# Kernel tuning notes

Measured on AMD Instinct MI355X. Metric: run time of the kernel, lower is better.

## Reference

```python
import jax, jax.numpy as jnp
import numpy as np

MAX_ITER = 10   # float32 branch of cg()
TOL = 1e-10

def _cdot(a, b):
    # complex_dot: sum(conj(a) * b) over all elements
    return jnp.sum(jnp.conj(a) * b)

def _A(p, smaps, mask):
    # p: [H,W] complex, smaps: [C,H,W] complex, mask: [H,W] real
    return jnp.fft.fft2(smaps * p[None], norm='ortho') * mask[None]

def _AH(y, smaps, mask):
    imgs = jnp.fft.ifft2(y * mask[None], norm='ortho')
    return jnp.sum(jnp.conj(smaps) * imgs, axis=0)  # [H,W]

def _cg(M, rhs):
    # conjugate gradient, faithful to the TF while_loop body
    def cond(s):
        i, rTr, x, r, p = s
        return jnp.logical_and(i < MAX_ITER, rTr > TOL)
    def body(s):
        i, rTr, x, r, p = s
        Ap = M(p)
        alpha = rTr / jnp.real(_cdot(p, Ap))
        x = x + p * alpha
        r = r - Ap * alpha
        rTrNew = jnp.real(_cdot(r, r))
        beta = rTrNew / rTr
        p = r + p * beta
        return (i + 1, rTrNew, x, r, p)
    rTr0 = jnp.real(_cdot(rhs, rhs))
    s0 = (jnp.int32(0), rTr0, jnp.zeros_like(rhs), rhs, rhs)
    return jax.lax.while_loop(cond, body, s0)[2]

def _solve_one(lambdaa, rhs, smaps, mask):
    M = lambda p: _AH(_A(p, smaps, mask), smaps, mask) + p * lambdaa
    return _cg(M, rhs)

_solve_b = jax.vmap(_solve_one, in_axes=(None, 0, 0, 0))  # replaces map_fn
_AH_b = jax.vmap(_AH, in_axes=(0, 0, 0))

def setup_inputs():
    key = jax.random.key(0)
    ks = jax.random.split(key, 7)
    B, C, H, W = 4, 16, 384, 384
    f = lambda k, s: jax.random.normal(k, s, dtype=jnp.float32)
    return {
        'lambdaa': 0.05 * jnp.ones((), jnp.float32),
        'x_re': f(ks[0], (B, H, W)),
        'x_im': f(ks[1], (B, H, W)),
        'y_re': f(ks[2], (B, C, H, W)),
        'y_im': f(ks[3], (B, C, H, W)),
        'smaps_re': f(ks[4], (B, C, H, W)),
        'smaps_im': f(ks[5], (B, C, H, W)),
        'mask': (jax.random.uniform(ks[6], (B, H, W)) < 0.33).astype(jnp.float32),
    }

def reference(lambdaa, x_re, x_im, y_re, y_im, smaps_re, smaps_im, mask):
    x = jax.lax.complex(x_re, x_im)
    y = jax.lax.complex(y_re, y_im)
    smaps = jax.lax.complex(smaps_re, smaps_im)
    # rhs = AH(y) + lambdaa * x
    rhs = _AH_b(y, smaps, mask) + x * lambdaa
    out = _solve_b(lambdaa, rhs, smaps, mask)  # [B,H,W] complex
    return jnp.stack([out.real, out.imag], axis=-1)  # [B,H,W,2] float32
```

## Files before the change

kernel.cpp:

```cpp
#include <hip/hip_runtime.h>
#include <hip/hip_fp16.h>


#define Bn 4
#define Cn 16
#define Hn 384
#define Wn 384
#define NPIX (Hn*Wn)
#define NPIX2 (NPIX/2)
#define TPB 256
#define CTPB 512
#define NCOL 16
#define TOLF 1e-10f
#define NITER 10
#define RED_BLKS 72
#define RPITCH 416
#define CPITCH 417

__device__ __forceinline__ float2 cadd(float2 a, float2 b){ return make_float2(a.x+b.x, a.y+b.y); }
__device__ __forceinline__ float2 csub(float2 a, float2 b){ return make_float2(a.x-b.x, a.y-b.y); }
__device__ __forceinline__ float2 cmulf(float2 a, float2 b){
  return make_float2(a.x*b.x - a.y*b.y, a.x*b.y + a.y*b.x);
}

__device__ __forceinline__ void wave_fence(){ asm volatile("s_waitcnt lgkmcnt(0)" ::: "memory"); }

template<int IMM>
__device__ __forceinline__ float2 shx(float2 v){
  int x = __builtin_amdgcn_ds_swizzle(__float_as_int(v.x), IMM);
  int y = __builtin_amdgcn_ds_swizzle(__float_as_int(v.y), IMM);
  return make_float2(__int_as_float(x), __int_as_float(y));
}

__device__ __forceinline__ int rev5(int x){
  return ((x&1)<<4) | ((x&2)<<2) | (x&4) | ((x&8)>>2) | ((x&16)>>4);
}

__device__ __forceinline__ int offmap(int w){ return w + ((w*683)>>13); }

template<int DIR>
__device__ __forceinline__ void fft12(float2* v)
{
  const float S3 = (DIR<0) ? -0.86602540378443864676f : 0.86602540378443864676f;
  const float sg = (DIR<0) ? -1.f : 1.f;
  float2 t[4][3];
#pragma unroll
  for (int b = 0; b < 4; ++b) {
    float2 a0 = v[b], a1 = v[4+b], a2 = v[8+b];
    float2 s = cadd(a1,a2), d = csub(a1,a2);
    float2 mm = make_float2(a0.x - 0.5f*s.x, a0.y - 0.5f*s.y);
    float2 e  = make_float2(-d.y*S3, d.x*S3);
    t[b][0] = cadd(a0,s);
    t[b][1] = cadd(mm,e);
    t[b][2] = csub(mm,e);
  }
  const float2 w1  = make_float2(0.86602540378443864676f, sg*0.5f);
  const float2 w2  = make_float2(0.5f, sg*0.86602540378443864676f);
  const float2 w3  = make_float2(0.f, sg);
  const float2 w4t = make_float2(-0.5f, sg*0.86602540378443864676f);
  const float2 w6  = make_float2(-1.f, 0.f);
  t[1][1] = cmulf(t[1][1], w1);  t[1][2] = cmulf(t[1][2], w2);
  t[2][1] = cmulf(t[2][1], w2);  t[2][2] = cmulf(t[2][2], w4t);
  t[3][1] = cmulf(t[3][1], w3);  t[3][2] = cmulf(t[3][2], w6);
#pragma unroll
  for (int c = 0; c < 3; ++c) {
    float2 e = cadd(t[0][c], t[2][c]);
    float2 f = csub(t[0][c], t[2][c]);
    float2 g = cadd(t[1][c], t[3][c]);
    float2 h = csub(t[1][c], t[3][c]);
    float2 ih = (DIR<0) ? make_float2(h.y, -h.x) : make_float2(-h.y, h.x);
    v[c]   = cadd(e,g);
    v[c+3] = cadd(f,ih);
    v[c+6] = csub(e,g);
    v[c+9] = csub(f,ih);
  }
}

template<int DIR>
__device__ __forceinline__ void fft32_lanes(float2* v, int li)
{
  const float c2pi = (DIR<0) ? -6.2831853071795864769f : 6.2831853071795864769f;
  const float sg   = (DIR<0) ? -1.f : 1.f;
  float s, c;
  __sincosf(c2pi*(1.f/32.f)*(float)(li&15), &s, &c); float2 wA = make_float2(c,s);
  __sincosf(c2pi*(1.f/16.f)*(float)(li&7),  &s, &c); float2 wB = make_float2(c,s);
  __sincosf(c2pi*(1.f/ 8.f)*(float)(li&3),  &s, &c); float2 wC = make_float2(c,s);
  bool bA = li & 16, bB = li & 8, bC = li & 4, bD = li & 2, bE = li & 1;
#pragma unroll
  for (int k = 0; k < 12; ++k) {
    float2 a = v[k], o;
    o = shx<0x401F>(a); a = bA ? cmulf(csub(o,a), wA) : cadd(a,o);
    o = shx<0x201F>(a); a = bB ? cmulf(csub(o,a), wB) : cadd(a,o);
    o = shx<0x101F>(a); a = bC ? cmulf(csub(o,a), wC) : cadd(a,o);
    o = shx<0x081F>(a);
    { float2 su = cadd(a,o), d = csub(o,a);
      float2 dw = bE ? make_float2(-sg*d.y, sg*d.x) : d;
      a = bD ? dw : su; }
    o = shx<0x041F>(a); a = bE ? csub(o,a) : cadd(a,o);
    v[k] = a;
  }
}

template<int DIR>
__device__ __forceinline__ void fft384(float2* v, int li)
{
  fft12<DIR>(v);
  const float c2pi = (DIR<0) ? -6.2831853071795864769f : 6.2831853071795864769f;
  float s, c;
  __sincosf(c2pi*(1.f/384.f)*(float)li, &s, &c);
  float2 W = make_float2(c,s), cw = W;
#pragma unroll
  for (int k = 1; k < 12; ++k) { v[k] = cmulf(v[k], cw); cw = cmulf(cw, W); }
  fft32_lanes<DIR>(v, li);
}


__global__ __launch_bounds__(TPB) void k_row_fwd(
    const float2* __restrict__ p, const float* __restrict__ Sre,
    const float* __restrict__ Sim, __half2* __restrict__ tmp)
{
  __shared__ float2 lbuf[8*RPITCH];
  int tid = threadIdx.x;
  int wave = tid>>6, lane = tid&63, sub = lane>>5, li = lane&31;
  int row = wave*2 + sub;
  int tile = blockIdx.x % (Hn/8);
  int bc   = blockIdx.x / (Hn/8);
  int b = bc / Cn;
  int h = tile*8 + row;
  size_t gbase = (size_t)bc*NPIX + (size_t)h*Wn;
  size_t pbase = (size_t)b*NPIX + (size_t)h*Wn;

  float2 v[12];
#pragma unroll
  for (int k = 0; k < 12; ++k) {
    int w = 32*k + li;
    float2 pv = p[pbase + w];
    float sr = Sre[gbase + w], si = Sim[gbase + w];
    v[k] = make_float2(sr*pv.x - si*pv.y, sr*pv.y + si*pv.x);
  }
  fft384<-1>(v, li);
  int m = rev5(li);
  float2* lrow = lbuf + row*RPITCH;
#pragma unroll
  for (int k = 0; k < 12; ++k) lrow[13*m + k] = v[k];
  wave_fence();
#pragma unroll
  for (int k = 0; k < 12; ++k) {
    int w = 32*k + li;
    tmp[gbase + w] = __float22half2_rn(lrow[offmap(w)]);
  }
}

template<int CPGt>
__global__ __launch_bounds__(TPB) void k_row_inv_acc(
    const __half2* __restrict__ tmp, const float* __restrict__ Sre,
    const float* __restrict__ Sim, float2* __restrict__ partial)
{
  const int GRPt = Cn/CPGt;
  __shared__ float2 lbuf[8*RPITCH];
  int tid = threadIdx.x;
  int wave = tid>>6, lane = tid&63, sub = lane>>5, li = lane&31;
  int row = wave*2 + sub;
  int tile = blockIdx.x % (Hn/8);
  int rest = blockIdx.x / (Hn/8);
  int g = rest % GRPt;
  int b = rest / GRPt;
  int h = tile*8 + row;
  int m = rev5(li);
  float2* lrow = lbuf + row*RPITCH;

  size_t gbase0 = ((size_t)b*Cn + g*CPGt)*NPIX + (size_t)h*Wn;
  __half2 hb[12];
#pragma unroll
  for (int k = 0; k < 12; ++k) hb[k] = tmp[gbase0 + 32*k + li];

  float2 acc[12];
#pragma unroll
  for (int k = 0; k < 12; ++k) acc[k] = make_float2(0.f, 0.f);

  for (int j = 0; j < CPGt; ++j) {
    size_t gb = gbase0 + (size_t)j*NPIX;
    float2 vc[12];
#pragma unroll
    for (int k = 0; k < 12; ++k) vc[k] = __half22float2(hb[k]);
    if (j + 1 < CPGt) {
      size_t gbn = gb + NPIX;
#pragma unroll
      for (int k = 0; k < 12; ++k) hb[k] = tmp[gbn + 32*k + li];
    }
    fft384<1>(vc, li);
    wave_fence();
#pragma unroll
    for (int k = 0; k < 12; ++k) lrow[13*m + k] = vc[k];
    wave_fence();
#pragma unroll
    for (int k = 0; k < 12; ++k) {
      int w = 32*k + li;
      float2 u = lrow[offmap(w)];
      float sr = Sre[gb + w], si = Sim[gb + w];
      acc[k].x += sr*u.x + si*u.y;
      acc[k].y += sr*u.y - si*u.x;
    }
  }
  size_t pbase = ((size_t)g*Bn + b)*NPIX + (size_t)h*Wn;
#pragma unroll
  for (int k = 0; k < 12; ++k) partial[pbase + 32*k + li] = acc[k];
}

__global__ __launch_bounds__(TPB) void k_maskp(
    const float* __restrict__ mask, float* __restrict__ maskP,
    float* __restrict__ scal)
{
  int idx = blockIdx.x*TPB + threadIdx.x;
  if (blockIdx.x == 0) scal[threadIdx.x] = 0.0f;
  if (idx >= Bn*NPIX) return;
  int k = idx % 12; int t = idx / 12;
  int li = t & 31; t >>= 5;
  int w = t % Wn;  int b = t / Wn;
  maskP[idx] = mask[((size_t)b*Hn + (k + 12*rev5(li)))*Wn + w] * (1.0f/(float)NPIX);
}

__global__ __launch_bounds__(CTPB) void k_col_full(
    __half2* __restrict__ tmp, const float* __restrict__ maskP)
{
  __shared__ float2 dbuf[NCOL*CPITCH];
  int tid = threadIdx.x;
  int wave = tid>>6, lane = tid&63, sub = lane>>5, li = lane&31;
  int col = wave*2 + sub;
  int tile = blockIdx.x % (Wn/NCOL);
  int bc   = blockIdx.x / (Wn/NCOL);
  int b = bc / Cn;
  int w0 = tile*NCOL;
  size_t tbase = (size_t)bc*NPIX;

  for (int e = tid; e < NCOL*Hn; e += CTPB) {
    int wi = e & (NCOL-1), h = e >> 4;
    dbuf[wi*CPITCH + offmap(h)] = __half22float2(tmp[tbase + (size_t)h*Wn + w0 + wi]);
  }
  __syncthreads();

  float2* drow = dbuf + col*CPITCH;
  int w = w0 + col;
  int m = rev5(li);
  const float4* mp4 = (const float4*)(maskP + (((size_t)b*Wn + w)*32 + li)*12);
  float4 m0 = mp4[0], m1 = mp4[1], m2 = mp4[2];
  float2 v[12];
#pragma unroll
  for (int k = 0; k < 12; ++k) v[k] = drow[offmap(32*k + li)];
  fft384<-1>(v, li);
  float mk[12] = {m0.x,m0.y,m0.z,m0.w, m1.x,m1.y,m1.z,m1.w, m2.x,m2.y,m2.z,m2.w};
#pragma unroll
  for (int k = 0; k < 12; ++k) v[k] = make_float2(v[k].x*mk[k], v[k].y*mk[k]);
  wave_fence();
#pragma unroll
  for (int k = 0; k < 12; ++k) drow[13*m + k] = v[k];
  wave_fence();
#pragma unroll
  for (int k = 0; k < 12; ++k) v[k] = drow[offmap(32*k + li)];
  fft384<1>(v, li);
  wave_fence();
#pragma unroll
  for (int k = 0; k < 12; ++k) drow[13*m + k] = v[k];
  __syncthreads();

  for (int e = tid; e < NCOL*Hn; e += CTPB) {
    int wi = e & (NCOL-1), h = e >> 4;
    tmp[tbase + (size_t)h*Wn + w0 + wi] = __float22half2_rn(dbuf[wi*CPITCH + offmap(h)]);
  }
}

__global__ __launch_bounds__(CTPB) void k_col_rhs(
    const float* __restrict__ yre, const float* __restrict__ yim,
    const float* __restrict__ mask, __half2* __restrict__ tmp)
{
  __shared__ float2 dbuf[NCOL*CPITCH];
  int tid = threadIdx.x;
  int wave = tid>>6, lane = tid&63, sub = lane>>5, li = lane&31;
  int col = wave*2 + sub;
  int tile = blockIdx.x % (Wn/NCOL);
  int bc   = blockIdx.x / (Wn/NCOL);
  int b = bc / Cn;
  int w0 = tile*NCOL;
  size_t tbase = (size_t)bc*NPIX;
  size_t mbase = (size_t)b*NPIX;

  for (int e = tid; e < NCOL*Hn; e += CTPB) {
    int wi = e & (NCOL-1), h = e >> 4;
    size_t gi = (size_t)h*Wn + w0 + wi;
    float mv = mask[mbase + gi] * (1.0f/384.0f);
    dbuf[wi*CPITCH + offmap(h)] = make_float2(yre[tbase+gi]*mv, yim[tbase+gi]*mv);
  }
  __syncthreads();

  float2* drow = dbuf + col*CPITCH;
  int m = rev5(li);
  float2 v[12];
#pragma unroll
  for (int k = 0; k < 12; ++k) v[k] = drow[offmap(32*k + li)];
  fft384<1>(v, li);
  wave_fence();
#pragma unroll
  for (int k = 0; k < 12; ++k) drow[13*m + k] = v[k];
  __syncthreads();

  for (int e = tid; e < NCOL*Hn; e += CTPB) {
    int wi = e & (NCOL-1), h = e >> 4;
    tmp[tbase + (size_t)h*Wn + w0 + wi] = __float22half2_rn(dbuf[wi*CPITCH + offmap(h)]);
  }
}


__device__ __forceinline__ void block_reduce_atomic(float sum, float* target)
{
  __shared__ float red[TPB];
  red[threadIdx.x] = sum; __syncthreads();
  for (int s = TPB/2; s > 0; s >>= 1) {
    if (threadIdx.x < s) red[threadIdx.x] += red[threadIdx.x + s];
    __syncthreads();
  }
  if (threadIdx.x == 0) unsafeAtomicAdd(target, red[0]);
  __syncthreads();
}

template<int GRPt>
__global__ __launch_bounds__(TPB) void k_rhs_init(
    const float* __restrict__ xre, const float* __restrict__ xim,
    const float* __restrict__ lam, const float2* __restrict__ partial,
    float2* __restrict__ r, float2* __restrict__ p, float2* __restrict__ x,
    float* __restrict__ scal)
{
  int b = blockIdx.y;
  float l = lam[0];
  float sum = 0.0f;
  const float2* xr2 = (const float2*)(xre + (size_t)b*NPIX);
  const float2* xi2 = (const float2*)(xim + (size_t)b*NPIX);
  float4* r4 = (float4*)(r + (size_t)b*NPIX);
  float4* p4 = (float4*)(p + (size_t)b*NPIX);
  float4* x4 = (float4*)(x + (size_t)b*NPIX);
  for (int i = blockIdx.x*TPB + threadIdx.x; i < NPIX2; i += RED_BLKS*TPB) {
    float2 re = xr2[i], im = xi2[i];
    float4 rv = make_float4(l*re.x, l*im.x, l*re.y, l*im.y);
#pragma unroll
    for (int g = 0; g < GRPt; ++g) {
      float4 pv = ((const float4*)(partial + ((size_t)g*Bn + b)*NPIX))[i];
      rv.x += pv.x; rv.y += pv.y; rv.z += pv.z; rv.w += pv.w;
    }
    r4[i] = rv; p4[i] = rv;
    x4[i] = make_float4(0.f, 0.f, 0.f, 0.f);
    sum += rv.x*rv.x + rv.y*rv.y + rv.z*rv.z + rv.w*rv.w;
  }
  block_reduce_atomic(sum, &scal[b]);
}

template<int GRPt>
__global__ __launch_bounds__(TPB) void k_combine_dot3(
    const float2* __restrict__ p, const float2* __restrict__ r,
    const float* __restrict__ lam, const float2* __restrict__ partial,
    float2* __restrict__ Ap, float* __restrict__ slot)
{
  int b = blockIdx.y;
  float l = lam[0];
  float s_pAp = 0.f, s_AA = 0.f, s_rA = 0.f;
  const float4* p4 = (const float4*)(p + (size_t)b*NPIX);
  const float4* r4 = (const float4*)(r + (size_t)b*NPIX);
  float4* A4 = (float4*)(Ap + (size_t)b*NPIX);
  for (int i = blockIdx.x*TPB + threadIdx.x; i < NPIX2; i += RED_BLKS*TPB) {
    float4 pv = p4[i];
    float4 av = make_float4(l*pv.x, l*pv.y, l*pv.z, l*pv.w);
#pragma unroll
    for (int g = 0; g < GRPt; ++g) {
      float4 qv = ((const float4*)(partial + ((size_t)g*Bn + b)*NPIX))[i];
      av.x += qv.x; av.y += qv.y; av.z += qv.z; av.w += qv.w;
    }
    A4[i] = av;
    float4 rv = r4[i];
    s_pAp += pv.x*av.x + pv.y*av.y + pv.z*av.z + pv.w*av.w;
    s_AA  += av.x*av.x + av.y*av.y + av.z*av.z + av.w*av.w;
    s_rA  += rv.x*av.x + rv.y*av.y + rv.z*av.z + rv.w*av.w;
  }
  block_reduce_atomic(s_pAp, &slot[b]);
  block_reduce_atomic(s_AA,  &slot[4+b]);
  block_reduce_atomic(s_rA,  &slot[8+b]);
}

__global__ void k_scal(float* __restrict__ scal, int it)
{
  int b = threadIdx.x;
  if (b >= Bn) return;
  float rtr = scal[it*4 + b];
  const float* slot = scal + 64 + it*12;
  float* ab = scal + 224 + it*12;
  bool act = rtr > TOLF;
  float alpha = act ? rtr / slot[b] : 0.f;
  float rtrn = act ? fmaxf(rtr - 2.f*alpha*slot[8+b] + alpha*alpha*slot[4+b], 0.f) : rtr;
  float beta = act ? rtrn / rtr : 0.f;
  scal[(it+1)*4 + b] = rtrn;
  ab[b] = alpha; ab[4+b] = beta; ab[8+b] = act ? 1.f : 0.f;
}

__global__ __launch_bounds__(TPB) void k_upd(
    float2* __restrict__ x, float2* __restrict__ r, float2* __restrict__ p,
    const float2* __restrict__ Ap, const float* __restrict__ ab)
{
  int b = blockIdx.y;
  if (!(ab[8+b] > 0.5f)) return;
  float alpha = ab[b], beta = ab[4+b];
  float4* x4 = (float4*)(x + (size_t)b*NPIX);
  float4* r4 = (float4*)(r + (size_t)b*NPIX);
  float4* p4 = (float4*)(p + (size_t)b*NPIX);
  const float4* A4 = (const float4*)(Ap + (size_t)b*NPIX);
  for (int i = blockIdx.x*TPB + threadIdx.x; i < NPIX2; i += RED_BLKS*TPB) {
    float4 pv = p4[i], av = A4[i], xv = x4[i], rv = r4[i];
    xv.x += alpha*pv.x; xv.y += alpha*pv.y; xv.z += alpha*pv.z; xv.w += alpha*pv.w;
    rv.x -= alpha*av.x; rv.y -= alpha*av.y; rv.z -= alpha*av.z; rv.w -= alpha*av.w;
    x4[i] = xv; r4[i] = rv;
    p4[i] = make_float4(rv.x + beta*pv.x, rv.y + beta*pv.y,
                        rv.z + beta*pv.z, rv.w + beta*pv.w);
  }
}


extern "C" void kernel_launch(void* const* d_in, const int* in_sizes, int n_in,
                              void* d_out, int out_size, void* d_ws, size_t ws_size,
                              hipStream_t stream)
{
  const float* lam  = (const float*)d_in[0];
  const float* xre  = (const float*)d_in[1];
  const float* xim  = (const float*)d_in[2];
  const float* yre  = (const float*)d_in[3];
  const float* yim  = (const float*)d_in[4];
  const float* sre  = (const float*)d_in[5];
  const float* sim  = (const float*)d_in[6];
  const float* mask = (const float*)d_in[7];

  const size_t szTmp  = (size_t)Bn*Cn*NPIX*sizeof(__half2);
  const size_t szVec  = (size_t)Bn*NPIX*sizeof(float2);
  const size_t szMask = (size_t)Bn*NPIX*sizeof(float);
  const size_t need8  = szTmp + 8*szVec + 3*szVec + 2048 + szMask;
  const int GRP = (ws_size >= need8) ? 8 : 4;

  char* ws = (char*)d_ws;
  __half2* tmp = (__half2*)ws;  ws += szTmp;
  float2* part = (float2*)ws;   ws += (size_t)GRP*szVec;
  float2* r    = (float2*)ws;   ws += szVec;
  float2* p    = (float2*)ws;   ws += szVec;
  float2* Ap   = (float2*)ws;   ws += szVec;
  float*  scal = (float*)ws;    ws += 2048;
  float*  mskP = (float*)ws;
  float2* x    = (float2*)d_out;

  dim3 blk(TPB);
  dim3 rg(RED_BLKS, Bn);
  int grid_row = Bn*Cn*(Hn/8);
  int grid_col = Bn*Cn*(Wn/NCOL);
  int grid_inv = Bn*GRP*(Hn/8);

  k_maskp<<<(Bn*NPIX)/TPB, blk, 0, stream>>>(mask, mskP, scal);

  k_col_rhs<<<grid_col, CTPB, 0, stream>>>(yre, yim, mask, tmp);
  if (GRP == 8) {
    k_row_inv_acc<2><<<grid_inv, blk, 0, stream>>>(tmp, sre, sim, part);
    k_rhs_init<8><<<rg, blk, 0, stream>>>(xre, xim, lam, part, r, p, x, scal);
  } else {
    k_row_inv_acc<4><<<grid_inv, blk, 0, stream>>>(tmp, sre, sim, part);
    k_rhs_init<4><<<rg, blk, 0, stream>>>(xre, xim, lam, part, r, p, x, scal);
  }

  for (int it = 0; it < NITER; ++it) {
    k_row_fwd<<<grid_row, blk, 0, stream>>>(p, sre, sim, tmp);
    k_col_full<<<grid_col, CTPB, 0, stream>>>(tmp, mskP);
    if (GRP == 8) {
      k_row_inv_acc<2><<<grid_inv, blk, 0, stream>>>(tmp, sre, sim, part);
      k_combine_dot3<8><<<rg, blk, 0, stream>>>(p, r, lam, part, Ap, scal + 64 + it*12);
    } else {
      k_row_inv_acc<4><<<grid_inv, blk, 0, stream>>>(tmp, sre, sim, part);
      k_combine_dot3<4><<<rg, blk, 0, stream>>>(p, r, lam, part, Ap, scal + 64 + it*12);
    }
    k_scal<<<1, 64, 0, stream>>>(scal, it);
    k_upd<<<rg, blk, 0, stream>>>(x, r, p, Ap, scal + 224 + it*12);
  }
}
```

Baseline: 1.580 ms.

## Keep CG-loop spectra in scrambled order and pack coil maps to half2

Inside the CG loop, the forward row FFT now writes its output in the FFT's natural scrambled order, with no LDS reorder. The column pass and the inverse row FFT then use a matching decimation-in-time FFT that accepts scrambled input and returns natural order. The mask permutation is adjusted to match the scrambled column index. This removes several LDS shuffles and fences per FFT. Separately, the coil sensitivity maps are packed once into a half2 buffer (when workspace allows) to halve their read traffic, at the cost of extra rounding error. Channel grouping is fixed at four groups instead of choosing eight when space allows.

```diff
diff --git a/kernel.cpp b/kernel.cpp
--- a/kernel.cpp
+++ b/kernel.cpp
@@ -14,6 +14,8 @@
 #define TOLF 1e-10f
 #define NITER 10
 #define RED_BLKS 72
+#define GRP 4
+#define CPG 4
 #define RPITCH 416
 #define CPITCH 417
 
@@ -102,6 +104,33 @@
 }
 
 template<int DIR>
+__device__ __forceinline__ void fft32_lanes_dit(float2* v, int li)
+{
+  const float c2pi = (DIR<0) ? -6.2831853071795864769f : 6.2831853071795864769f;
+  const float sg   = (DIR<0) ? -1.f : 1.f;
+  float s, c;
+  __sincosf(c2pi*(1.f/32.f)*(float)(li&15), &s, &c); float2 wA = make_float2(c,s);
+  __sincosf(c2pi*(1.f/16.f)*(float)(li&7),  &s, &c); float2 wB = make_float2(c,s);
+  __sincosf(c2pi*(1.f/ 8.f)*(float)(li&3),  &s, &c); float2 wC = make_float2(c,s);
+  bool bA = li & 16, bB = li & 8, bC = li & 4, bD = li & 2, bE = li & 1;
+#pragma unroll
+  for (int k = 0; k < 12; ++k) {
+    float2 a = v[k], o;
+    o = shx<0x041F>(a); a = bE ? csub(o,a) : cadd(a,o);
+    { float2 aw = make_float2(-sg*a.y, sg*a.x);
+      a = (bD && bE) ? aw : a;
+      o = shx<0x081F>(a); a = bD ? csub(o,a) : cadd(a,o); }
+    { float2 aw = cmulf(a, wC); a = bC ? aw : a;
+      o = shx<0x101F>(a); a = bC ? csub(o,a) : cadd(a,o); }
+    { float2 aw = cmulf(a, wB); a = bB ? aw : a;
+      o = shx<0x201F>(a); a = bB ? csub(o,a) : cadd(a,o); }
+    { float2 aw = cmulf(a, wA); a = bA ? aw : a;
+      o = shx<0x401F>(a); a = bA ? csub(o,a) : cadd(a,o); }
+    v[k] = a;
+  }
+}
+
+template<int DIR>
 __device__ __forceinline__ void fft384(float2* v, int li)
 {
   fft12<DIR>(v);
@@ -114,12 +143,26 @@
   fft32_lanes<DIR>(v, li);
 }
 
-
+template<int DIR>
+__device__ __forceinline__ void fft384_scr(float2* v, int li)
+{
+  fft32_lanes_dit<DIR>(v, li);
+  const float c2pi = (DIR<0) ? -6.2831853071795864769f : 6.2831853071795864769f;
+  float s, c;
+  __sincosf(c2pi*(1.f/384.f)*(float)li, &s, &c);
+  float2 W = make_float2(c,s), cw = W;
+#pragma unroll
+  for (int k = 1; k < 12; ++k) { v[k] = cmulf(v[k], cw); cw = cmulf(cw, W); }
+  fft12<DIR>(v);
+}
+
+
+template<bool HS>
 __global__ __launch_bounds__(TPB) void k_row_fwd(
     const float2* __restrict__ p, const float* __restrict__ Sre,
-    const float* __restrict__ Sim, __half2* __restrict__ tmp)
-{
-  __shared__ float2 lbuf[8*RPITCH];
+    const float* __restrict__ Sim, const __half2* __restrict__ Sh,
+    __half2* __restrict__ tmp)
+{
   int tid = threadIdx.x;
   int wave = tid>>6, lane = tid&63, sub = lane>>5, li = lane&31;
   int row = wave*2 + sub;
@@ -135,41 +178,84 @@
   for (int k = 0; k < 12; ++k) {
     int w = 32*k + li;
     float2 pv = p[pbase + w];
-    float sr = Sre[gbase + w], si = Sim[gbase + w];
+    float sr, si;
+    if (HS) { float2 sv = __half22float2(Sh[gbase + w]); sr = sv.x; si = sv.y; }
+    else    { sr = Sre[gbase + w]; si = Sim[gbase + w]; }
     v[k] = make_float2(sr*pv.x - si*pv.y, sr*pv.y + si*pv.x);
   }
   fft384<-1>(v, li);
-  int m = rev5(li);
-  float2* lrow = lbuf + row*RPITCH;
-#pragma unroll
-  for (int k = 0; k < 12; ++k) lrow[13*m + k] = v[k];
-  wave_fence();
-#pragma unroll
-  for (int k = 0; k < 12; ++k) {
-    int w = 32*k + li;
-    tmp[gbase + w] = __float22half2_rn(lrow[offmap(w)]);
-  }
-}
-
-template<int CPGt>
-__global__ __launch_bounds__(TPB) void k_row_inv_acc(
+#pragma unroll
+  for (int k = 0; k < 12; ++k)
+    tmp[gbase + 32*k + li] = __float22half2_rn(v[k]);
+}
+
+template<bool HS>
+__global__ __launch_bounds__(TPB) void k_row_inv_scr(
+    const __half2* __restrict__ tmp, const float* __restrict__ Sre,
+    const float* __restrict__ Sim, const __half2* __restrict__ Sh,
+    float2* __restrict__ partial)
+{
+  int tid = threadIdx.x;
+  int wave = tid>>6, lane = tid&63, sub = lane>>5, li = lane&31;
+  int row = wave*2 + sub;
+  int tile = blockIdx.x % (Hn/8);
+  int rest = blockIdx.x / (Hn/8);
+  int g = rest % GRP;
+  int b = rest / GRP;
+  int h = tile*8 + row;
+
+  size_t gbase0 = ((size_t)b*Cn + g*CPG)*NPIX + (size_t)h*Wn;
+  __half2 hb[12];
+#pragma unroll
+  for (int k = 0; k < 12; ++k) hb[k] = tmp[gbase0 + 32*k + li];
+
+  float2 acc[12];
+#pragma unroll
+  for (int k = 0; k < 12; ++k) acc[k] = make_float2(0.f, 0.f);
+
+  for (int j = 0; j < CPG; ++j) {
+    size_t gb = gbase0 + (size_t)j*NPIX;
+    float2 vc[12];
+#pragma unroll
+    for (int k = 0; k < 12; ++k) vc[k] = __half22float2(hb[k]);
+    if (j + 1 < CPG) {
+      size_t gbn = gb + NPIX;
+#pragma unroll
+      for (int k = 0; k < 12; ++k) hb[k] = tmp[gbn + 32*k + li];
+    }
+    fft384_scr<1>(vc, li);
+#pragma unroll
+    for (int k = 0; k < 12; ++k) {
+      int w = 32*k + li;
+      float sr, si;
+      if (HS) { float2 sv = __half22float2(Sh[gb + w]); sr = sv.x; si = sv.y; }
+      else    { sr = Sre[gb + w]; si = Sim[gb + w]; }
+      acc[k].x += sr*vc[k].x + si*vc[k].y;
+      acc[k].y += sr*vc[k].y - si*vc[k].x;
+    }
+  }
+  size_t pbase = ((size_t)g*Bn + b)*NPIX + (size_t)h*Wn;
+#pragma unroll
+  for (int k = 0; k < 12; ++k) partial[pbase + 32*k + li] = acc[k];
+}
+
+__global__ __launch_bounds__(TPB) void k_row_inv_nat(
     const __half2* __restrict__ tmp, const float* __restrict__ Sre,
     const float* __restrict__ Sim, float2* __restrict__ partial)
 {
-  const int GRPt = Cn/CPGt;
   __shared__ float2 lbuf[8*RPITCH];
   int tid = threadIdx.x;
   int wave = tid>>6, lane = tid&63, sub = lane>>5, li = lane&31;
   int row = wave*2 + sub;
   int tile = blockIdx.x % (Hn/8);
   int rest = blockIdx.x / (Hn/8);
-  int g = rest % GRPt;
-  int b = rest / GRPt;
+  int g = rest % GRP;
+  int b = rest / GRP;
   int h = tile*8 + row;
   int m = rev5(li);
   float2* lrow = lbuf + row*RPITCH;
 
-  size_t gbase0 = ((size_t)b*Cn + g*CPGt)*NPIX + (size_t)h*Wn;
+  size_t gbase0 = ((size_t)b*Cn + g*CPG)*NPIX + (size_t)h*Wn;
   __half2 hb[12];
 #pragma unroll
   for (int k = 0; k < 12; ++k) hb[k] = tmp[gbase0 + 32*k + li];
@@ -178,12 +264,12 @@
 #pragma unroll
   for (int k = 0; k < 12; ++k) acc[k] = make_float2(0.f, 0.f);
 
-  for (int j = 0; j < CPGt; ++j) {
+  for (int j = 0; j < CPG; ++j) {
     size_t gb = gbase0 + (size_t)j*NPIX;
     float2 vc[12];
 #pragma unroll
     for (int k = 0; k < 12; ++k) vc[k] = __half22float2(hb[k]);
-    if (j + 1 < CPGt) {
+    if (j + 1 < CPG) {
       size_t gbn = gb + NPIX;
 #pragma unroll
       for (int k = 0; k < 12; ++k) hb[k] = tmp[gbn + 32*k + li];
@@ -207,6 +293,14 @@
   for (int k = 0; k < 12; ++k) partial[pbase + 32*k + li] = acc[k];
 }
 
+__global__ __launch_bounds__(TPB) void k_spack(
+    const float* __restrict__ sre, const float* __restrict__ sim,
+    __half2* __restrict__ sh)
+{
+  size_t i = (size_t)blockIdx.x*TPB + threadIdx.x;
+  if (i < (size_t)Bn*Cn*NPIX) sh[i] = __floats2half2_rn(sre[i], sim[i]);
+}
+
 __global__ __launch_bounds__(TPB) void k_maskp(
     const float* __restrict__ mask, float* __restrict__ maskP,
     float* __restrict__ scal)
@@ -216,8 +310,9 @@
   if (idx >= Bn*NPIX) return;
   int k = idx % 12; int t = idx / 12;
   int li = t & 31; t >>= 5;
-  int w = t % Wn;  int b = t / Wn;
-  maskP[idx] = mask[((size_t)b*Hn + (k + 12*rev5(li)))*Wn + w] * (1.0f/(float)NPIX);
+  int wa = t % Wn; int b = t / Wn;
+  int wt = (wa >> 5) + 12*rev5(wa & 31);
+  maskP[idx] = mask[((size_t)b*Hn + (k + 12*rev5(li)))*Wn + wt] * (1.0f/(float)NPIX);
 }
 
 __global__ __launch_bounds__(CTPB) void k_col_full(
@@ -241,7 +336,6 @@
 
   float2* drow = dbuf + col*CPITCH;
   int w = w0 + col;
-  int m = rev5(li);
   const float4* mp4 = (const float4*)(maskP + (((size_t)b*Wn + w)*32 + li)*12);
   float4 m0 = mp4[0], m1 = mp4[1], m2 = mp4[2];
   float2 v[12];
@@ -251,16 +345,9 @@
   float mk[12] = {m0.x,m0.y,m0.z,m0.w, m1.x,m1.y,m1.z,m1.w, m2.x,m2.y,m2.z,m2.w};
 #pragma unroll
   for (int k = 0; k < 12; ++k) v[k] = make_float2(v[k].x*mk[k], v[k].y*mk[k]);
-  wave_fence();
-#pragma unroll
-  for (int k = 0; k < 12; ++k) drow[13*m + k] = v[k];
-  wave_fence();
-#pragma unroll
-  for (int k = 0; k < 12; ++k) v[k] = drow[offmap(32*k + li)];
-  fft384<1>(v, li);
-  wave_fence();
-#pragma unroll
-  for (int k = 0; k < 12; ++k) drow[13*m + k] = v[k];
+  fft384_scr<1>(v, li);
+#pragma unroll
+  for (int k = 0; k < 12; ++k) drow[offmap(32*k + li)] = v[k];
   __syncthreads();
 
   for (int e = tid; e < NCOL*Hn; e += CTPB) {
@@ -322,7 +409,6 @@
   __syncthreads();
 }
 
-template<int GRPt>
 __global__ __launch_bounds__(TPB) void k_rhs_init(
     const float* __restrict__ xre, const float* __restrict__ xim,
     const float* __restrict__ lam, const float2* __restrict__ partial,
@@ -341,7 +427,7 @@
     float2 re = xr2[i], im = xi2[i];
     float4 rv = make_float4(l*re.x, l*im.x, l*re.y, l*im.y);
 #pragma unroll
-    for (int g = 0; g < GRPt; ++g) {
+    for (int g = 0; g < GRP; ++g) {
       float4 pv = ((const float4*)(partial + ((size_t)g*Bn + b)*NPIX))[i];
       rv.x += pv.x; rv.y += pv.y; rv.z += pv.z; rv.w += pv.w;
     }
@@ -352,7 +438,6 @@
   block_reduce_atomic(sum, &scal[b]);
 }
 
-template<int GRPt>
 __global__ __launch_bounds__(TPB) void k_combine_dot3(
     const float2* __restrict__ p, const float2* __restrict__ r,
     const float* __restrict__ lam, const float2* __restrict__ partial,
@@ -368,7 +453,7 @@
     float4 pv = p4[i];
     float4 av = make_float4(l*pv.x, l*pv.y, l*pv.z, l*pv.w);
 #pragma unroll
-    for (int g = 0; g < GRPt; ++g) {
+    for (int g = 0; g < GRP; ++g) {
       float4 qv = ((const float4*)(partial + ((size_t)g*Bn + b)*NPIX))[i];
       av.x += qv.x; av.y += qv.y; av.z += qv.z; av.w += qv.w;
     }
@@ -436,8 +521,9 @@
   const size_t szTmp  = (size_t)Bn*Cn*NPIX*sizeof(__half2);
   const size_t szVec  = (size_t)Bn*NPIX*sizeof(float2);
   const size_t szMask = (size_t)Bn*NPIX*sizeof(float);
-  const size_t need8  = szTmp + 8*szVec + 3*szVec + 2048 + szMask;
-  const int GRP = (ws_size >= need8) ? 8 : 4;
+  const size_t szSh   = (size_t)Bn*Cn*NPIX*sizeof(__half2);
+  const size_t base   = szTmp + (size_t)GRP*szVec + 3*szVec + 2048 + szMask;
+  const bool useSh    = (ws_size >= base + szSh);
 
   char* ws = (char*)d_ws;
   __half2* tmp = (__half2*)ws;  ws += szTmp;
@@ -446,7 +532,8 @@
   float2* p    = (float2*)ws;   ws += szVec;
   float2* Ap   = (float2*)ws;   ws += szVec;
   float*  scal = (float*)ws;    ws += 2048;
-  float*  mskP = (float*)ws;
+  float*  mskP = (float*)ws;    ws += szMask;
+  __half2* Sh  = (__half2*)ws;
   float2* x    = (float2*)d_out;
 
   dim3 blk(TPB);
@@ -456,26 +543,24 @@
   int grid_inv = Bn*GRP*(Hn/8);
 
   k_maskp<<<(Bn*NPIX)/TPB, blk, 0, stream>>>(mask, mskP, scal);
+  if (useSh)
+    k_spack<<<(Bn*Cn*NPIX)/TPB, blk, 0, stream>>>(sre, sim, Sh);
 
   k_col_rhs<<<grid_col, CTPB, 0, stream>>>(yre, yim, mask, tmp);
-  if (GRP == 8) {
-    k_row_inv_acc<2><<<grid_inv, blk, 0, stream>>>(tmp, sre, sim, part);
-    k_rhs_init<8><<<rg, blk, 0, stream>>>(xre, xim, lam, part, r, p, x, scal);
-  } else {
-    k_row_inv_acc<4><<<grid_inv, blk, 0, stream>>>(tmp, sre, sim, part);
-    k_rhs_init<4><<<rg, blk, 0, stream>>>(xre, xim, lam, part, r, p, x, scal);
-  }
+  k_row_inv_nat<<<grid_inv, blk, 0, stream>>>(tmp, sre, sim, part);
+  k_rhs_init<<<rg, blk, 0, stream>>>(xre, xim, lam, part, r, p, x, scal);
 
   for (int it = 0; it < NITER; ++it) {
-    k_row_fwd<<<grid_row, blk, 0, stream>>>(p, sre, sim, tmp);
-    k_col_full<<<grid_col, CTPB, 0, stream>>>(tmp, mskP);
-    if (GRP == 8) {
-      k_row_inv_acc<2><<<grid_inv, blk, 0, stream>>>(tmp, sre, sim, part);
-      k_combine_dot3<8><<<rg, blk, 0, stream>>>(p, r, lam, part, Ap, scal + 64 + it*12);
+    if (useSh) {
+      k_row_fwd<true><<<grid_row, blk, 0, stream>>>(p, sre, sim, Sh, tmp);
+      k_col_full<<<grid_col, CTPB, 0, stream>>>(tmp, mskP);
+      k_row_inv_scr<true><<<grid_inv, blk, 0, stream>>>(tmp, sre, sim, Sh, part);
     } else {
-      k_row_inv_acc<4><<<grid_inv, blk, 0, stream>>>(tmp, sre, sim, part);
-      k_combine_dot3<4><<<rg, blk, 0, stream>>>(p, r, lam, part, Ap, scal + 64 + it*12);
-    }
+      k_row_fwd<false><<<grid_row, blk, 0, stream>>>(p, sre, sim, Sh, tmp);
+      k_col_full<<<grid_col, CTPB, 0, stream>>>(tmp, mskP);
+      k_row_inv_scr<false><<<grid_inv, blk, 0, stream>>>(tmp, sre, sim, Sh, part);
+    }
+    k_combine_dot3<<<rg, blk, 0, stream>>>(p, r, lam, part, Ap, scal + 64 + it*12);
     k_scal<<<1, 64, 0, stream>>>(scal, it);
     k_upd<<<rg, blk, 0, stream>>>(x, r, p, Ap, scal + 224 + it*12);
   }
```

Result: faster. 1.470 ms (-6.9%).
